# Performance work log

Measured on AMD Instinct MI355X. Metric: run time of the kernel, lower is better.

The kernel has to match this reference:

```python
import jax, jax.numpy as jnp
import numpy as np

B, H, S, W, F = 16, 4, 8, 256, 16


def setup_inputs() -> dict:
    key = jax.random.key(0)
    kx, kk = jax.random.split(key)
    x = jax.random.normal(kx, (B, S, W, F), dtype=jnp.float32)
    kernel = jax.random.normal(kk, (H, S, S, W), dtype=jnp.float32)
    return {"x": x, "kernel": kernel}


def reference(x, kernel):
    # kernel: [H, S, S, W]; x: [B, S, W, F]
    Hh, Ss, _, Ww = kernel.shape
    r = jnp.arange(Ww)
    # stacked[h,x,y,j,i] = roll(kernel, shifts=j+1)[i] = kernel[(i-(j+1)) % W]
    idx = (r[None, :] - (r[:, None] + 1)) % Ww          # [W(row=j), W(col=i)]
    stacked = kernel[..., idx]                            # [H,S,S,W,W]
    # torch.tril over last two dims: keep col i <= row j
    tri = (r[None, :] <= r[:, None])                      # [W,W]
    stacked = jnp.where(tri, stacked, jnp.zeros((), dtype=stacked.dtype))
    # masked triangular time-mix contraction
    out = jnp.einsum('hxyji,bxif->bhxyjf', stacked, x)    # [B,H,S,S,W,F]
    base = jnp.arange(1, Ww + 1, dtype=out.dtype).reshape(1, 1, 1, 1, Ww, 1)
    out = out / base
    # transform_x: on diagonal series (x==y) roll time dim by 1, zero first step
    diag_mod = jnp.roll(out, 1, axis=4)
    not_first = (r != 0).reshape(1, 1, 1, 1, Ww, 1)
    diag_mod = diag_mod * not_first.astype(out.dtype)
    eye = jnp.eye(Ss, dtype=bool).reshape(1, 1, Ss, Ss, 1, 1)
    return jnp.where(eye, diag_mod, out)
```

## Files before the change

kernel.cpp:

```cpp
#include <hip/hip_runtime.h>
#include <hip/hip_bf16.h>

typedef short short8 __attribute__((ext_vector_type(8)));
typedef float f32x4 __attribute__((ext_vector_type(4)));

union FragAB { unsigned long long l[2]; int i[4]; short8 v; };

__global__ __launch_bounds__(256, 4)
void k_fused(const float* __restrict__ x,
             const float* __restrict__ kern,
             float* __restrict__ out)
{
    __shared__ __align__(16) ushort Xts[64 * 264];
    __shared__ __align__(8)  ushort wforL[4][336];
    __shared__ float rtab[256];

    const int blk = blockIdx.x;
    const int hy = blk & 31;
    const int sx = (blk >> 5) & 7;
    const int nt = blk >> 8;
    const int h = hy >> 3, sy = hy & 7;
    const int diag = (sx == sy) ? 1 : 0;
    const int t = threadIdx.x;

    {
        const float* krow = kern + ((h * 8 + sx) * 8 + sy) * 256;
        #pragma unroll
        for (int s = 0; s < 4; ++s) {
            #pragma unroll
            for (int pass = 0; pass < 2; ++pass) {
                int q = t + pass * 256;
                if (q < 336) {
                    int src = q - s;
                    float v = (src >= 0 && src < 256) ? krow[src] : 0.0f;
                    __hip_bfloat16 hv = __float2bfloat16(v);
                    wforL[s][q] = reinterpret_cast<ushort&>(hv);
                }
            }
        }
    }
    {
        int denom = t + 1 - diag;
        rtab[t] = (denom > 0) ? (1.0f / (float)denom) : 0.0f;
    }
    {
        const float4* xbase = reinterpret_cast<const float4*>(x);
        #pragma unroll
        for (int it = 0; it < 8; ++it) {
            int id = it * 256 + t;
            int fq = id & 3;
            int k2 = (id >> 2) & 127;
            int bl = id >> 9;
            const float4* rowp = xbase + ((size_t)((nt * 4 + bl) * 8 + sx)) * 1024;
            float4 a = rowp[(2 * k2) * 4 + fq];
            float4 cq = rowp[(2 * k2 + 1) * 4 + fq];
            #pragma unroll
            for (int e = 0; e < 4; ++e) {
                float va = (&a.x)[e], vb = (&cq.x)[e];
                __hip_bfloat16 ha = __float2bfloat16(va);
                __hip_bfloat16 hb = __float2bfloat16(vb);
                uint u = (uint)reinterpret_cast<ushort&>(ha) |
                         ((uint)reinterpret_cast<ushort&>(hb) << 16);
                int row = bl * 16 + fq * 4 + e;
                *reinterpret_cast<uint*>(reinterpret_cast<char*>(Xts) + row * 528 + k2 * 4) = u;
            }
        }
    }
    __syncthreads();

    const int lane = t & 63, wid = t >> 6;
    const int laneM = lane & 15, laneG = lane >> 4;
    const int wb = wid * 16;

    const char* XtsB = reinterpret_cast<const char*>(Xts);
    const char* WB = reinterpret_cast<const char*>(wforL);
    const int abyte = laneM * 528 + laneG * 16;

    const int w000 = 255 + diag - wb - laneM + 8 * laneG;
    const int s = (laneM - diag + 1) & 3;
    const int bB0 = s * 674 + 2 * w000;

    f32x4 acc[4][4];
    #pragma unroll
    for (int g = 0; g < 4; ++g)
        #pragma unroll
        for (int m = 0; m < 4; ++m)
            acc[g][m] = (f32x4){0.0f, 0.0f, 0.0f, 0.0f};

    const int kend = wb + 208;
    for (int kc = 0; kc < kend; kc += 32) {
        FragAB af[4];
        #pragma unroll
        for (int m = 0; m < 4; ++m) {
            const int4 raw = *reinterpret_cast<const int4*>(XtsB + abyte + m * 8448 + kc * 2);
            af[m].i[0] = raw.x; af[m].i[1] = raw.y;
            af[m].i[2] = raw.z; af[m].i[3] = raw.w;
        }
        #pragma unroll
        for (int g = 0; g < 4; ++g) {
            const int kmaxg = wb + 64 * g + 16;
            if (kc < kmaxg) {
                FragAB bf;
                {
                    const char* p = WB + (bB0 - 128 * g) + kc * 2;
                    bf.l[0] = *reinterpret_cast<const unsigned long long*>(p);
                    bf.l[1] = *reinterpret_cast<const unsigned long long*>(p + 8);
                }
                #pragma unroll
                for (int m = 0; m < 4; ++m)
                    acc[g][m] = __builtin_amdgcn_mfma_f32_16x16x32_bf16(
                        af[m].v, bf.v, acc[g][m], 0, 0, 0);
                if (kc + 32 >= kmaxg) {
                    const int j = wb + 64 * g + laneM;
                    const float rt = rtab[j];
                    #pragma unroll
                    for (int m = 0; m < 4; ++m) {
                        const int b_ = nt * 4 + m;
                        float* dst = out
                            + (((size_t)(b_ * 4 + h) * 8 + sx) * 8 + sy) * 4096
                            + (size_t)j * 16 + laneG * 4;
                        f32x4 v = acc[g][m] * rt;
                        __builtin_nontemporal_store(v, reinterpret_cast<f32x4*>(dst));
                    }
                }
            }
        }
    }
}

extern "C" void kernel_launch(void* const* d_in, const int* in_sizes, int n_in,
                              void* d_out, int out_size, void* d_ws, size_t ws_size,
                              hipStream_t stream) {
    const float* x    = (const float*)d_in[0];
    const float* kern = (const float*)d_in[1];
    float* out = (float*)d_out;

    k_fused<<<1024, 256, 0, stream>>>(x, kern, out);
}
```

Before: 20.67 us.

## Repartition warp work across batch pairs and interleaved time tiles for load balance

```diff
diff --git a/kernel.cpp b/kernel.cpp
--- a/kernel.cpp
+++ b/kernel.cpp
@@ -6,7 +6,7 @@
 
 union FragAB { unsigned long long l[2]; int i[4]; short8 v; };
 
-__global__ __launch_bounds__(256, 4)
+__global__ __launch_bounds__(256, 3)
 void k_fused(const float* __restrict__ x,
              const float* __restrict__ kern,
              float* __restrict__ out)
@@ -70,58 +70,58 @@
 
     const int lane = t & 63, wid = t >> 6;
     const int laneM = lane & 15, laneG = lane >> 4;
-    const int wb = wid * 16;
+    const int wp  = wid >> 1;
+    const int par = wid & 1;
 
     const char* XtsB = reinterpret_cast<const char*>(Xts);
     const char* WB = reinterpret_cast<const char*>(wforL);
-    const int abyte = laneM * 528 + laneG * 16;
+    const int abyte = (32 * wp + laneM) * 528 + laneG * 16;
 
-    const int w000 = 255 + diag - wb - laneM + 8 * laneG;
-    const int s = (laneM - diag + 1) & 3;
-    const int bB0 = s * 674 + 2 * w000;
+    const int w00 = 255 + diag - 16 * par - laneM + 8 * laneG;
+    const int s = (laneM - diag + 1 - 16 * par) & 3;
+    const int bBw = s * 674 + 2 * w00;
 
-    f32x4 acc[4][4];
+    f32x4 acc[8][2];
     #pragma unroll
-    for (int g = 0; g < 4; ++g)
+    for (int g = 0; g < 8; ++g)
         #pragma unroll
-        for (int m = 0; m < 4; ++m)
+        for (int m = 0; m < 2; ++m)
             acc[g][m] = (f32x4){0.0f, 0.0f, 0.0f, 0.0f};
 
-    const int kend = wb + 208;
-    for (int kc = 0; kc < kend; kc += 32) {
-        FragAB af[4];
+    #pragma unroll
+    for (int st = 0; st < 8; ++st) {
+        const int kc = 32 * st;
+        FragAB af[2];
         #pragma unroll
-        for (int m = 0; m < 4; ++m) {
-            const int4 raw = *reinterpret_cast<const int4*>(XtsB + abyte + m * 8448 + kc * 2);
+        for (int m = 0; m < 2; ++m) {
+            const int4 raw = *reinterpret_cast<const int4*>(
+                XtsB + abyte + m * 8448 + kc * 2);
             af[m].i[0] = raw.x; af[m].i[1] = raw.y;
             af[m].i[2] = raw.z; af[m].i[3] = raw.w;
         }
         #pragma unroll
-        for (int g = 0; g < 4; ++g) {
-            const int kmaxg = wb + 64 * g + 16;
-            if (kc < kmaxg) {
+        for (int g = 0; g < 8; ++g) {
+            if (g >= st) {
                 FragAB bf;
-                {
-                    const char* p = WB + (bB0 - 128 * g) + kc * 2;
-                    bf.l[0] = *reinterpret_cast<const unsigned long long*>(p);
-                    bf.l[1] = *reinterpret_cast<const unsigned long long*>(p + 8);
-                }
+                const char* p = WB + bBw - 64 * g + kc * 2;
+                bf.l[0] = *reinterpret_cast<const unsigned long long*>(p);
+                bf.l[1] = *reinterpret_cast<const unsigned long long*>(p + 8);
                 #pragma unroll
-                for (int m = 0; m < 4; ++m)
+                for (int m = 0; m < 2; ++m)
                     acc[g][m] = __builtin_amdgcn_mfma_f32_16x16x32_bf16(
                         af[m].v, bf.v, acc[g][m], 0, 0, 0);
-                if (kc + 32 >= kmaxg) {
-                    const int j = wb + 64 * g + laneM;
-                    const float rt = rtab[j];
-                    #pragma unroll
-                    for (int m = 0; m < 4; ++m) {
-                        const int b_ = nt * 4 + m;
-                        float* dst = out
-                            + (((size_t)(b_ * 4 + h) * 8 + sx) * 8 + sy) * 4096
-                            + (size_t)j * 16 + laneG * 4;
-                        f32x4 v = acc[g][m] * rt;
-                        __builtin_nontemporal_store(v, reinterpret_cast<f32x4*>(dst));
-                    }
+            }
+            if (g == st) {
+                const int j = 32 * g + 16 * par + laneM;
+                const float rt = rtab[j];
+                #pragma unroll
+                for (int m = 0; m < 2; ++m) {
+                    const int b_ = nt * 4 + 2 * wp + m;
+                    float* dst = out
+                        + (((size_t)(b_ * 4 + h) * 8 + sx) * 8 + sy) * 4096
+                        + (size_t)j * 16 + laneG * 4;
+                    f32x4 v = acc[g][m] * rt;
+                    __builtin_nontemporal_store(v, reinterpret_cast<f32x4*>(dst));
                 }
             }
         }
```

Result: no change. 20.69 us (+0.1%).
